# Performance work log

Measured on AMD Instinct MI355X. Metric: run time of the kernel, lower is better.

## Reference

```python
import jax, jax.numpy as jnp
import numpy as np
import math

DIM = 512
B, T, H, W = 1, 8, 64, 64


def setup_inputs() -> dict:
    key = jax.random.key(0)
    k0, k1, k2 = jax.random.split(key, 3)
    x = jax.random.normal(k0, (B, DIM, T, H, W), dtype=jnp.float32)
    gamma = jnp.ones((DIM,), jnp.float32)                      # RMS_norm gamma (viewed as flat vector)
    w_qkv = jax.random.normal(k1, (3 * DIM, DIM), jnp.float32) * 0.02  # conv1x1 weight (out, in)
    b_qkv = jnp.zeros((3 * DIM,), jnp.float32)
    w_proj = jax.random.normal(k2, (DIM, DIM), jnp.float32) * 0.02     # zero-init in torch; random for a meaningful baseline
    b_proj = jnp.zeros((DIM,), jnp.float32)
    return dict(x=x, gamma=gamma, w_qkv=w_qkv, b_qkv=b_qkv, w_proj=w_proj, b_proj=b_proj)


def reference(x, gamma, w_qkv, b_qkv, w_proj, b_proj):
    b, c, t, h, w = x.shape
    xt = jnp.transpose(x, (0, 2, 3, 4, 1))          # [b, t, h, w, c]
    identity = xt
    y = xt.reshape(b * t, h, w, c)
    # RMS_norm: L2 norm over channels (last dim), clamped, scaled by sqrt(c)*gamma
    norm = jnp.clip(jnp.linalg.norm(y, axis=-1, keepdims=True), 1e-12, None)
    y = y / norm * (c ** 0.5) * gamma
    # 1x1 conv QKV as GEMM over channels
    qkv = jnp.einsum('bhwc,oc->bhwo', y, w_qkv) + b_qkv        # [bt, h, w, 3c]
    qkv = qkv.reshape(b * t, h * w, 1, 3 * c)                  # nh=1 per source rearrange
    q, k, v = jnp.split(qkv, 3, axis=-1)                       # each [bt, hw, 1, c]
    scale = 1.0 / math.sqrt(c)
    # NOTE: hw sits in the batch position (faithful to source); seq len = nh = 1
    attn = jnp.einsum('bsnc,bsmc->bsnm', q, k) * scale         # [bt, hw, 1, 1]
    attn = jax.nn.softmax(attn, axis=-1)                       # trivially 1.0
    o = jnp.einsum('bsnm,bsmc->bsnc', attn, v)                 # == v
    o = o.reshape(b * t, h, w, c)
    o = jnp.einsum('bhwc,oc->bhwo', o, w_proj) + b_proj        # 1x1 proj conv
    o = o.reshape(b, t, h, w, c)
    out = jnp.transpose(o + identity, (0, 4, 1, 2, 3))         # back to [b, c, t, h, w]
    return out
```

## Files before the change

### kernel.cpp

```cpp
#include <hip/hip_runtime.h>

typedef unsigned short ushort_t;
typedef __attribute__((ext_vector_type(8))) short short8;
typedef __attribute__((ext_vector_type(4))) float f32x4;

#define DIMC 512
#define PN   32768
#define SQRTC 22.627416997969522f

__device__ __forceinline__ ushort_t f2bf(float f) {
  unsigned int u = __float_as_uint(f);
  unsigned int r = u + 0x7fffu + ((u >> 16) & 1u);
  return (ushort_t)(r >> 16);
}

__device__ __forceinline__ int kkey(int r) { return (r & 7) ^ ((r >> 2) & 7); }

__global__ __launch_bounds__(256) void k_prep(const float* __restrict__ wproj,
                                              const float* __restrict__ wqkv,
                                              const float* __restrict__ bqkv,
                                              const float* __restrict__ bproj,
                                              ushort_t* __restrict__ wpb,
                                              ushort_t* __restrict__ WvT,
                                              float* __restrict__ fb) {
  int bid = blockIdx.x, tid = threadIdx.x;
  if (bid < 256) {
    int i = (bid * 256 + tid) * 4;
    float4 v = *(const float4*)(wproj + i);
    ushort_t o[4] = {f2bf(v.x), f2bf(v.y), f2bf(v.z), f2bf(v.w)};
    *(uint2*)(wpb + i) = *(const uint2*)o;
  } else if (bid < 384) {
    int c = (bid - 256) * 4 + (tid >> 6);
    int k8 = (tid & 63) * 8;
    ushort_t tmp[8];
#pragma unroll
    for (int j = 0; j < 8; ++j)
      tmp[j] = f2bf(wqkv[(long)(1024 + k8 + j) * DIMC + c]);
    *(uint4*)(WvT + (long)c * DIMC + k8) = *(const uint4*)tmp;
  } else {
    int wave = tid >> 6, lane = tid & 63;
    int o = (bid - 384) * 4 + wave;
    float part = 0.f;
#pragma unroll
    for (int i = 0; i < 8; ++i) {
      int k = lane + i * 64;
      part += wproj[o * DIMC + k] * bqkv[1024 + k];
    }
    for (int off = 32; off; off >>= 1) part += __shfl_down(part, off, 64);
    if (lane == 0) fb[o] = part + bproj[o];
  }
}

__global__ __launch_bounds__(256) void k_gemm_w(
    const ushort_t* __restrict__ A,
    const ushort_t* __restrict__ BT,
    ushort_t* __restrict__ C,
    const float* __restrict__ gamma) {
  __shared__ ushort_t As[128 * 64];
  __shared__ ushort_t Bs[128 * 64];
  int tid = threadIdx.x;
  int p0 = blockIdx.x * 128;
  int o0 = blockIdx.y * 128;
  int wave = tid >> 6, lane = tid & 63;
  int wo = (wave & 1) * 64, wp = (wave >> 1) * 64;
  int q = lane >> 4, ln = lane & 15;

  f32x4 zero = {0.f, 0.f, 0.f, 0.f};
  f32x4 acc[4][4];
#pragma unroll
  for (int i = 0; i < 4; ++i)
#pragma unroll
    for (int j = 0; j < 4; ++j) acc[i][j] = zero;

  int sr = tid >> 3;
  int sc = tid & 7;
  const ushort_t* Ag = A + (long)(o0 + sr) * DIMC + sc * 8;
  const ushort_t* Bg = BT + (long)(p0 + sr) * DIMC + sc * 8;

  for (int kc = 0; kc < DIMC; kc += 64) {
    __syncthreads();
#pragma unroll
    for (int it = 0; it < 4; ++it) {
      int r = sr + it * 32;
      uint4 va = *(const uint4*)(Ag + (long)it * 32 * DIMC + kc);
      uint4 vb = *(const uint4*)(Bg + (long)it * 32 * DIMC + kc);
      int sw = ((sc ^ (r & 7)) * 8);
      *(uint4*)(&As[r * 64 + sw]) = va;
      *(uint4*)(&Bs[r * 64 + sw]) = vb;
    }
    __syncthreads();
#pragma unroll
    for (int ks = 0; ks < 2; ++ks) {
      int cch = ks * 4 + q;
      short8 af[4], bf[4];
#pragma unroll
      for (int mi = 0; mi < 4; ++mi) {
        int row = wo + mi * 16 + ln;
        af[mi] = *(const short8*)(&As[row * 64 + ((cch ^ (row & 7)) * 8)]);
      }
#pragma unroll
      for (int ni = 0; ni < 4; ++ni) {
        int row = wp + ni * 16 + ln;
        bf[ni] = *(const short8*)(&Bs[row * 64 + ((cch ^ (row & 7)) * 8)]);
      }
#pragma unroll
      for (int mi = 0; mi < 4; ++mi)
#pragma unroll
        for (int ni = 0; ni < 4; ++ni)
          acc[mi][ni] = __builtin_amdgcn_mfma_f32_16x16x32_bf16(af[mi], bf[ni], acc[mi][ni], 0, 0, 0);
    }
  }

#pragma unroll
  for (int mi = 0; mi < 4; ++mi) {
    int obase = o0 + wo + mi * 16 + q * 4;
#pragma unroll
    for (int ni = 0; ni < 4; ++ni) {
      int c = p0 + wp + ni * 16 + ln;
      float g = gamma[c];
      int kb2 = c >> 6, ks2 = (c >> 5) & 1, q2 = (c >> 3) & 3, j2 = c & 7;
#pragma unroll
      for (int r = 0; r < 4; ++r) {
        int o = obase + r;
        int w2 = o >> 6, mi2 = (o >> 4) & 3, ln2 = o & 15;
        long idx = (((((long)w2 * 8 + kb2) * 2 + ks2) * 4 + mi2) * 64 + q2 * 16 + ln2) * 8 + j2;
        C[idx] = f2bf(acc[mi][ni][r] * g);
      }
    }
  }
}

__global__ __launch_bounds__(512, 4) void k_fused(
    const float* __restrict__ x,
    const ushort_t* __restrict__ Mp2,
    const float* __restrict__ fb,
    float* __restrict__ out) {
  __shared__ ushort_t xs[8 * 64 * 64];
  __shared__ float red[32 * 65];
  __shared__ float s_sh[64];
  int tid = threadIdx.x;
  long p0 = (long)blockIdx.x * 64;

  int wave = tid >> 6, lane = tid & 63;
  int q = lane >> 4, ln = lane & 15;

  const ushort_t* Aw = Mp2 + (long)wave * 32768 + lane * 8;
  short8 a0[8];
#pragma unroll
  for (int f = 0; f < 8; ++f) a0[f] = *(const short8*)(Aw + f * 512);

  int pl4 = (tid & 15) * 4;
  int kq  = tid >> 4;
  float ss0 = 0.f, ss1 = 0.f, ss2 = 0.f, ss3 = 0.f;
#pragma unroll
  for (int sw = 0; sw < 4; ++sw) {
    int k4 = kq * 4 + sw * 128;
    const float* xp = x + (long)k4 * PN + p0 + pl4;
    float4 v0 = *(const float4*)(xp);
    float4 v1 = *(const float4*)(xp + PN);
    float4 v2 = *(const float4*)(xp + 2 * PN);
    float4 v3 = *(const float4*)(xp + 3 * PN);
    ss0 += v0.x * v0.x + v1.x * v1.x + v2.x * v2.x + v3.x * v3.x;
    ss1 += v0.y * v0.y + v1.y * v1.y + v2.y * v2.y + v3.y * v3.y;
    ss2 += v0.z * v0.z + v1.z * v1.z + v2.z * v2.z + v3.z * v3.z;
    ss3 += v0.w * v0.w + v1.w * v1.w + v2.w * v2.w + v3.w * v3.w;
    ushort_t t0[4] = {f2bf(v0.x), f2bf(v1.x), f2bf(v2.x), f2bf(v3.x)};
    ushort_t t1[4] = {f2bf(v0.y), f2bf(v1.y), f2bf(v2.y), f2bf(v3.y)};
    ushort_t t2[4] = {f2bf(v0.z), f2bf(v1.z), f2bf(v2.z), f2bf(v3.z)};
    ushort_t t3[4] = {f2bf(v0.w), f2bf(v1.w), f2bf(v2.w), f2bf(v3.w)};
    char* base = (char*)xs + (k4 >> 6) * 8192;
    int ch  = (k4 >> 3) & 7;
    int sub = (k4 & 7) * 2;
    *(uint2*)(base + (pl4 + 0) * 128 + ((ch ^ kkey(pl4 + 0)) * 16) + sub) = *(const uint2*)t0;
    *(uint2*)(base + (pl4 + 1) * 128 + ((ch ^ kkey(pl4 + 1)) * 16) + sub) = *(const uint2*)t1;
    *(uint2*)(base + (pl4 + 2) * 128 + ((ch ^ kkey(pl4 + 2)) * 16) + sub) = *(const uint2*)t2;
    *(uint2*)(base + (pl4 + 3) * 128 + ((ch ^ kkey(pl4 + 3)) * 16) + sub) = *(const uint2*)t3;
  }
  red[kq * 65 + pl4 + 0] = ss0;
  red[kq * 65 + pl4 + 1] = ss1;
  red[kq * 65 + pl4 + 2] = ss2;
  red[kq * 65 + pl4 + 3] = ss3;
  __syncthreads();
  if (tid < 64) {
    float t = 0.f;
#pragma unroll
    for (int g = 0; g < 32; ++g) t += red[g * 65 + tid];
    s_sh[tid] = SQRTC / fmaxf(sqrtf(t), 1e-12f);
  }
  __syncthreads();

  f32x4 zero = {0.f, 0.f, 0.f, 0.f};
  f32x4 acc[4][4];
#pragma unroll
  for (int i = 0; i < 4; ++i)
#pragma unroll
    for (int j = 0; j < 4; ++j) acc[i][j] = zero;

#pragma unroll
  for (int kb = 0; kb < 8; ++kb) {
    const char* bbase = (const char*)xs + kb * 8192;
#pragma unroll
    for (int ks = 0; ks < 2; ++ks) {
      short8 af[4], bf[4];
#pragma unroll
      for (int mi = 0; mi < 4; ++mi)
        af[mi] = (kb == 0) ? a0[ks * 4 + mi]
                           : *(const short8*)(Aw + ((kb * 2 + ks) * 4 + mi) * 512);
      int cch = ks * 4 + q;
#pragma unroll
      for (int ni = 0; ni < 4; ++ni) {
        int row = ni * 16 + ln;
        bf[ni] = *(const short8*)(bbase + row * 128 + ((cch ^ kkey(row)) * 16));
      }
#pragma unroll
      for (int mi = 0; mi < 4; ++mi)
#pragma unroll
        for (int ni = 0; ni < 4; ++ni)
          acc[mi][ni] = __builtin_amdgcn_mfma_f32_16x16x32_bf16(af[mi], bf[ni], acc[mi][ni], 0, 0, 0);
    }
  }

  int wo = wave * 64;
#pragma unroll
  for (int mi = 0; mi < 4; ++mi) {
    int obase = wo + mi * 16 + q * 4;
#pragma unroll
    for (int ni = 0; ni < 4; ++ni) {
      int plocal = ni * 16 + ln;
      long p = p0 + plocal;
      float sv = s_sh[plocal];
#pragma unroll
      for (int r = 0; r < 4; ++r) {
        int o = obase + r;
        out[(long)o * PN + p] = x[(long)o * PN + p] + fb[o] + sv * acc[mi][ni][r];
      }
    }
  }
}

extern "C" void kernel_launch(void* const* d_in, const int* in_sizes, int n_in,
                              void* d_out, int out_size, void* d_ws, size_t ws_size,
                              hipStream_t stream) {
  const float* x     = (const float*)d_in[0];
  const float* gamma = (const float*)d_in[1];
  const float* wqkv  = (const float*)d_in[2];
  const float* bqkv  = (const float*)d_in[3];
  const float* wproj = (const float*)d_in[4];
  const float* bproj = (const float*)d_in[5];

  char* ws = (char*)d_ws;
  ushort_t* Mp2 = (ushort_t*)(ws);
  ushort_t* wpb = (ushort_t*)(ws + 524288);
  ushort_t* WvT = (ushort_t*)(ws + 1048576);
  float*    fb  = (float*)(ws + 1572864);

  k_prep<<<dim3(512), dim3(256), 0, stream>>>(wproj, wqkv, bqkv, bproj, wpb, WvT, fb);
  k_gemm_w<<<dim3(4, 4), dim3(256), 0, stream>>>(wpb, WvT, Mp2, gamma);
  k_fused<<<dim3(512), dim3(512), 0, stream>>>(x, Mp2, fb, (float*)d_out);
}
```

Before: 163.6 us.

## Fuse weight prep into GEMM kernel and pipeline x loads in fused kernel

```diff
diff --git a/kernel.cpp b/kernel.cpp
--- a/kernel.cpp
+++ b/kernel.cpp
@@ -16,30 +16,25 @@
 
 __device__ __forceinline__ int kkey(int r) { return (r & 7) ^ ((r >> 2) & 7); }
 
-__global__ __launch_bounds__(256) void k_prep(const float* __restrict__ wproj,
-                                              const float* __restrict__ wqkv,
-                                              const float* __restrict__ bqkv,
-                                              const float* __restrict__ bproj,
-                                              ushort_t* __restrict__ wpb,
-                                              ushort_t* __restrict__ WvT,
-                                              float* __restrict__ fb) {
+__device__ __forceinline__ uint4 pack8(float4 a, float4 b) {
+  union { ushort_t u[8]; uint4 v; } r;
+  r.u[0] = f2bf(a.x); r.u[1] = f2bf(a.y); r.u[2] = f2bf(a.z); r.u[3] = f2bf(a.w);
+  r.u[4] = f2bf(b.x); r.u[5] = f2bf(b.y); r.u[6] = f2bf(b.z); r.u[7] = f2bf(b.w);
+  return r.v;
+}
+
+__global__ __launch_bounds__(256) void k_wgemm(
+    const float* __restrict__ wproj,
+    const float* __restrict__ wqkv,
+    const float* __restrict__ bqkv,
+    const float* __restrict__ bproj,
+    const float* __restrict__ gamma,
+    ushort_t* __restrict__ Mp2,
+    float* __restrict__ fb) {
   int bid = blockIdx.x, tid = threadIdx.x;
-  if (bid < 256) {
-    int i = (bid * 256 + tid) * 4;
-    float4 v = *(const float4*)(wproj + i);
-    ushort_t o[4] = {f2bf(v.x), f2bf(v.y), f2bf(v.z), f2bf(v.w)};
-    *(uint2*)(wpb + i) = *(const uint2*)o;
-  } else if (bid < 384) {
-    int c = (bid - 256) * 4 + (tid >> 6);
-    int k8 = (tid & 63) * 8;
-    ushort_t tmp[8];
-#pragma unroll
-    for (int j = 0; j < 8; ++j)
-      tmp[j] = f2bf(wqkv[(long)(1024 + k8 + j) * DIMC + c]);
-    *(uint4*)(WvT + (long)c * DIMC + k8) = *(const uint4*)tmp;
-  } else {
+  if (bid >= 16) {
     int wave = tid >> 6, lane = tid & 63;
-    int o = (bid - 384) * 4 + wave;
+    int o = (bid - 16) * 4 + wave;
     float part = 0.f;
 #pragma unroll
     for (int i = 0; i < 8; ++i) {
@@ -48,19 +43,13 @@
     }
     for (int off = 32; off; off >>= 1) part += __shfl_down(part, off, 64);
     if (lane == 0) fb[o] = part + bproj[o];
-  }
-}
-
-__global__ __launch_bounds__(256) void k_gemm_w(
-    const ushort_t* __restrict__ A,
-    const ushort_t* __restrict__ BT,
-    ushort_t* __restrict__ C,
-    const float* __restrict__ gamma) {
+    return;
+  }
+
   __shared__ ushort_t As[128 * 64];
   __shared__ ushort_t Bs[128 * 64];
-  int tid = threadIdx.x;
-  int p0 = blockIdx.x * 128;
-  int o0 = blockIdx.y * 128;
+  int c0 = (bid & 3) * 128;
+  int o0 = (bid >> 2) * 128;
   int wave = tid >> 6, lane = tid & 63;
   int wo = (wave & 1) * 64, wp = (wave >> 1) * 64;
   int q = lane >> 4, ln = lane & 15;
@@ -74,19 +63,30 @@
 
   int sr = tid >> 3;
   int sc = tid & 7;
-  const ushort_t* Ag = A + (long)(o0 + sr) * DIMC + sc * 8;
-  const ushort_t* Bg = BT + (long)(p0 + sr) * DIMC + sc * 8;
+  const float* Ag = wproj + (long)(o0 + sr) * DIMC + sc * 8;
+  int kr = tid >> 5;
+  int c4 = (tid & 31) * 4;
 
   for (int kc = 0; kc < DIMC; kc += 64) {
     __syncthreads();
 #pragma unroll
     for (int it = 0; it < 4; ++it) {
       int r = sr + it * 32;
-      uint4 va = *(const uint4*)(Ag + (long)it * 32 * DIMC + kc);
-      uint4 vb = *(const uint4*)(Bg + (long)it * 32 * DIMC + kc);
-      int sw = ((sc ^ (r & 7)) * 8);
-      *(uint4*)(&As[r * 64 + sw]) = va;
-      *(uint4*)(&Bs[r * 64 + sw]) = vb;
+      float4 a0 = *(const float4*)(Ag + (long)it * 32 * DIMC + kc);
+      float4 a1 = *(const float4*)(Ag + (long)it * 32 * DIMC + kc + 4);
+      *(uint4*)(&As[r * 64 + ((sc ^ (r & 7)) * 8)]) = pack8(a0, a1);
+    }
+#pragma unroll
+    for (int ps = 0; ps < 8; ++ps) {
+      int k = kc + ps * 8 + kr;
+      float4 b = *(const float4*)(wqkv + (long)(1024 + k) * DIMC + c0 + c4);
+      char* bsb = (char*)Bs;
+      ushort_t e[4] = {f2bf(b.x), f2bf(b.y), f2bf(b.z), f2bf(b.w)};
+#pragma unroll
+      for (int i = 0; i < 4; ++i) {
+        int c = c4 + i;
+        *(ushort_t*)(bsb + c * 128 + ((ps ^ kkey(c)) * 16) + kr * 2) = e[i];
+      }
     }
     __syncthreads();
 #pragma unroll
@@ -101,7 +101,7 @@
 #pragma unroll
       for (int ni = 0; ni < 4; ++ni) {
         int row = wp + ni * 16 + ln;
-        bf[ni] = *(const short8*)(&Bs[row * 64 + ((cch ^ (row & 7)) * 8)]);
+        bf[ni] = *(const short8*)(&Bs[row * 64 + ((cch ^ kkey(row)) * 8)]);
       }
 #pragma unroll
       for (int mi = 0; mi < 4; ++mi)
@@ -116,7 +116,7 @@
     int obase = o0 + wo + mi * 16 + q * 4;
 #pragma unroll
     for (int ni = 0; ni < 4; ++ni) {
-      int c = p0 + wp + ni * 16 + ln;
+      int c = c0 + wp + ni * 16 + ln;
       float g = gamma[c];
       int kb2 = c >> 6, ks2 = (c >> 5) & 1, q2 = (c >> 3) & 3, j2 = c & 7;
 #pragma unroll
@@ -124,108 +124,124 @@
         int o = obase + r;
         int w2 = o >> 6, mi2 = (o >> 4) & 3, ln2 = o & 15;
         long idx = (((((long)w2 * 8 + kb2) * 2 + ks2) * 4 + mi2) * 64 + q2 * 16 + ln2) * 8 + j2;
-        C[idx] = f2bf(acc[mi][ni][r] * g);
-      }
-    }
-  }
-}
-
-__global__ __launch_bounds__(512, 4) void k_fused(
+        Mp2[idx] = f2bf(acc[mi][ni][r] * g);
+      }
+    }
+  }
+}
+
+__global__ __launch_bounds__(512, 6) void k_fused(
     const float* __restrict__ x,
     const ushort_t* __restrict__ Mp2,
     const float* __restrict__ fb,
     float* __restrict__ out) {
-  __shared__ ushort_t xs[8 * 64 * 64];
-  __shared__ float red[32 * 65];
-  __shared__ float s_sh[64];
+  __shared__ ushort_t xs[2 * 32 * 128];
+  __shared__ float red[8 * 32];
+  __shared__ float s_sh[32];
   int tid = threadIdx.x;
-  long p0 = (long)blockIdx.x * 64;
+  long p0 = (long)blockIdx.x * 32;
 
   int wave = tid >> 6, lane = tid & 63;
   int q = lane >> 4, ln = lane & 15;
 
+  int pi4 = (lane & 7) * 4;
+  int kq  = tid >> 3;
+  const float* xbase = x + p0 + pi4;
+  int ch = kq >> 2;
+  int sb = (kq & 3) * 4;
+
   const ushort_t* Aw = Mp2 + (long)wave * 32768 + lane * 8;
-  short8 a0[8];
-#pragma unroll
-  for (int f = 0; f < 8; ++f) a0[f] = *(const short8*)(Aw + f * 512);
-
-  int pl4 = (tid & 15) * 4;
-  int kq  = tid >> 4;
+
   float ss0 = 0.f, ss1 = 0.f, ss2 = 0.f, ss3 = 0.f;
-#pragma unroll
-  for (int sw = 0; sw < 4; ++sw) {
-    int k4 = kq * 4 + sw * 128;
-    const float* xp = x + (long)k4 * PN + p0 + pl4;
-    float4 v0 = *(const float4*)(xp);
-    float4 v1 = *(const float4*)(xp + PN);
-    float4 v2 = *(const float4*)(xp + 2 * PN);
-    float4 v3 = *(const float4*)(xp + 3 * PN);
-    ss0 += v0.x * v0.x + v1.x * v1.x + v2.x * v2.x + v3.x * v3.x;
-    ss1 += v0.y * v0.y + v1.y * v1.y + v2.y * v2.y + v3.y * v3.y;
-    ss2 += v0.z * v0.z + v1.z * v1.z + v2.z * v2.z + v3.z * v3.z;
-    ss3 += v0.w * v0.w + v1.w * v1.w + v2.w * v2.w + v3.w * v3.w;
-    ushort_t t0[4] = {f2bf(v0.x), f2bf(v1.x), f2bf(v2.x), f2bf(v3.x)};
-    ushort_t t1[4] = {f2bf(v0.y), f2bf(v1.y), f2bf(v2.y), f2bf(v3.y)};
-    ushort_t t2[4] = {f2bf(v0.z), f2bf(v1.z), f2bf(v2.z), f2bf(v3.z)};
-    ushort_t t3[4] = {f2bf(v0.w), f2bf(v1.w), f2bf(v2.w), f2bf(v3.w)};
-    char* base = (char*)xs + (k4 >> 6) * 8192;
-    int ch  = (k4 >> 3) & 7;
-    int sub = (k4 & 7) * 2;
-    *(uint2*)(base + (pl4 + 0) * 128 + ((ch ^ kkey(pl4 + 0)) * 16) + sub) = *(const uint2*)t0;
-    *(uint2*)(base + (pl4 + 1) * 128 + ((ch ^ kkey(pl4 + 1)) * 16) + sub) = *(const uint2*)t1;
-    *(uint2*)(base + (pl4 + 2) * 128 + ((ch ^ kkey(pl4 + 2)) * 16) + sub) = *(const uint2*)t2;
-    *(uint2*)(base + (pl4 + 3) * 128 + ((ch ^ kkey(pl4 + 3)) * 16) + sub) = *(const uint2*)t3;
-  }
-  red[kq * 65 + pl4 + 0] = ss0;
-  red[kq * 65 + pl4 + 1] = ss1;
-  red[kq * 65 + pl4 + 2] = ss2;
-  red[kq * 65 + pl4 + 3] = ss3;
+  float4 u0, u1;
+
+#define LOADX(T)                                                   \
+  { const float* xp = xbase + (long)((T) * 128 + kq * 2) * PN;     \
+    u0 = *(const float4*)(xp);  u1 = *(const float4*)(xp + PN); }
+
+#define SSW(B)                                                                  \
+  { ss0 += u0.x * u0.x + u1.x * u1.x;  ss1 += u0.y * u0.y + u1.y * u1.y;        \
+    ss2 += u0.z * u0.z + u1.z * u1.z;  ss3 += u0.w * u0.w + u1.w * u1.w;        \
+    unsigned int w0 = (unsigned int)f2bf(u0.x) | ((unsigned int)f2bf(u1.x) << 16); \
+    unsigned int w1 = (unsigned int)f2bf(u0.y) | ((unsigned int)f2bf(u1.y) << 16); \
+    unsigned int w2 = (unsigned int)f2bf(u0.z) | ((unsigned int)f2bf(u1.z) << 16); \
+    unsigned int w3 = (unsigned int)f2bf(u0.w) | ((unsigned int)f2bf(u1.w) << 16); \
+    char* bb = (char*)xs + (B) * 8192;                                          \
+    *(unsigned int*)(bb + (pi4 + 0) * 256 + ((ch ^ kkey(pi4 + 0)) * 16) + sb) = w0; \
+    *(unsigned int*)(bb + (pi4 + 1) * 256 + ((ch ^ kkey(pi4 + 1)) * 16) + sb) = w1; \
+    *(unsigned int*)(bb + (pi4 + 2) * 256 + ((ch ^ kkey(pi4 + 2)) * 16) + sb) = w2; \
+    *(unsigned int*)(bb + (pi4 + 3) * 256 + ((ch ^ kkey(pi4 + 3)) * 16) + sb) = w3; }
+
+  f32x4 zero = {0.f, 0.f, 0.f, 0.f};
+  f32x4 acc[4][2];
+#pragma unroll
+  for (int i = 0; i < 4; ++i)
+#pragma unroll
+    for (int j = 0; j < 2; ++j) acc[i][j] = zero;
+
+  LOADX(0); SSW(0);
   __syncthreads();
-  if (tid < 64) {
+
+#pragma unroll
+  for (int t = 0; t < 4; ++t) {
+    if (t < 3) LOADX(t + 1);
+    const char* bb = (const char*)xs + (t & 1) * 8192;
+#pragma unroll
+    for (int kbl = 0; kbl < 2; ++kbl) {
+      int kb = t * 2 + kbl;
+#pragma unroll
+      for (int ks = 0; ks < 2; ++ks) {
+        short8 af[4], bf[2];
+#pragma unroll
+        for (int mi = 0; mi < 4; ++mi)
+          af[mi] = *(const short8*)(Aw + ((kb * 2 + ks) * 4 + mi) * 512);
+        int c16 = kbl * 8 + ks * 4 + q;
+#pragma unroll
+        for (int ni = 0; ni < 2; ++ni) {
+          int row = ni * 16 + ln;
+          bf[ni] = *(const short8*)(bb + row * 256 + ((c16 ^ kkey(row)) * 16));
+        }
+#pragma unroll
+        for (int mi = 0; mi < 4; ++mi)
+#pragma unroll
+          for (int ni = 0; ni < 2; ++ni)
+            acc[mi][ni] = __builtin_amdgcn_mfma_f32_16x16x32_bf16(af[mi], bf[ni], acc[mi][ni], 0, 0, 0);
+      }
+    }
+    if (t < 3) {
+      SSW((t + 1) & 1);
+      __syncthreads();
+    }
+  }
+
+#pragma unroll
+  for (int m = 8; m <= 32; m <<= 1) {
+    ss0 += __shfl_xor(ss0, m, 64);
+    ss1 += __shfl_xor(ss1, m, 64);
+    ss2 += __shfl_xor(ss2, m, 64);
+    ss3 += __shfl_xor(ss3, m, 64);
+  }
+  if ((lane & 56) == 0) {
+    red[wave * 32 + pi4 + 0] = ss0;
+    red[wave * 32 + pi4 + 1] = ss1;
+    red[wave * 32 + pi4 + 2] = ss2;
+    red[wave * 32 + pi4 + 3] = ss3;
+  }
+  __syncthreads();
+  if (tid < 32) {
     float t = 0.f;
 #pragma unroll
-    for (int g = 0; g < 32; ++g) t += red[g * 65 + tid];
+    for (int g = 0; g < 8; ++g) t += red[g * 32 + tid];
     s_sh[tid] = SQRTC / fmaxf(sqrtf(t), 1e-12f);
   }
   __syncthreads();
-
-  f32x4 zero = {0.f, 0.f, 0.f, 0.f};
-  f32x4 acc[4][4];
-#pragma unroll
-  for (int i = 0; i < 4; ++i)
-#pragma unroll
-    for (int j = 0; j < 4; ++j) acc[i][j] = zero;
-
-#pragma unroll
-  for (int kb = 0; kb < 8; ++kb) {
-    const char* bbase = (const char*)xs + kb * 8192;
-#pragma unroll
-    for (int ks = 0; ks < 2; ++ks) {
-      short8 af[4], bf[4];
-#pragma unroll
-      for (int mi = 0; mi < 4; ++mi)
-        af[mi] = (kb == 0) ? a0[ks * 4 + mi]
-                           : *(const short8*)(Aw + ((kb * 2 + ks) * 4 + mi) * 512);
-      int cch = ks * 4 + q;
-#pragma unroll
-      for (int ni = 0; ni < 4; ++ni) {
-        int row = ni * 16 + ln;
-        bf[ni] = *(const short8*)(bbase + row * 128 + ((cch ^ kkey(row)) * 16));
-      }
-#pragma unroll
-      for (int mi = 0; mi < 4; ++mi)
-#pragma unroll
-        for (int ni = 0; ni < 4; ++ni)
-          acc[mi][ni] = __builtin_amdgcn_mfma_f32_16x16x32_bf16(af[mi], bf[ni], acc[mi][ni], 0, 0, 0);
-    }
-  }
 
   int wo = wave * 64;
 #pragma unroll
   for (int mi = 0; mi < 4; ++mi) {
     int obase = wo + mi * 16 + q * 4;
 #pragma unroll
-    for (int ni = 0; ni < 4; ++ni) {
+    for (int ni = 0; ni < 2; ++ni) {
       int plocal = ni * 16 + ln;
       long p = p0 + plocal;
       float sv = s_sh[plocal];
@@ -236,6 +252,8 @@
       }
     }
   }
+#undef LOADX
+#undef SSW
 }
 
 extern "C" void kernel_launch(void* const* d_in, const int* in_sizes, int n_in,
@@ -250,11 +268,8 @@
 
   char* ws = (char*)d_ws;
   ushort_t* Mp2 = (ushort_t*)(ws);
-  ushort_t* wpb = (ushort_t*)(ws + 524288);
-  ushort_t* WvT = (ushort_t*)(ws + 1048576);
-  float*    fb  = (float*)(ws + 1572864);
-
-  k_prep<<<dim3(512), dim3(256), 0, stream>>>(wproj, wqkv, bqkv, bproj, wpb, WvT, fb);
-  k_gemm_w<<<dim3(4, 4), dim3(256), 0, stream>>>(wpb, WvT, Mp2, gamma);
-  k_fused<<<dim3(512), dim3(512), 0, stream>>>(x, Mp2, fb, (float*)d_out);
-}
+  float*    fb  = (float*)(ws + 524288);
+
+  k_wgemm<<<dim3(144), dim3(256), 0, stream>>>(wproj, wqkv, bqkv, bproj, gamma, Mp2, fb);
+  k_fused<<<dim3(1024), dim3(512), 0, stream>>>(x, Mp2, fb, (float*)d_out);
+}
```

Result: slower. 213.5 us (+30.5%).
